# Optimization experiments

Hardware: AMD Instinct MI355X
Metric: run time of the kernel (lower is better)

The kernel has to match this reference:

```python
import jax, jax.numpy as jnp
import numpy as np
import math

DIM = 1024
HEADS = 16
SEQ_LEN = 2048
NUM_PV = 32
HEAD_DIM = DIM // HEADS
EPS = 1e-5


def setup_inputs() -> dict:
    key = jax.random.key(0)
    k1, k2 = jax.random.split(key)
    B = 4
    L = SEQ_LEN + NUM_PV
    x = jax.random.normal(k1, (B, L, DIM), dtype=jnp.float32)
    paramvecs = jax.random.normal(k2, (1, NUM_PV, DIM), dtype=jnp.float32)
    return {"x": x, "paramvecs": paramvecs}


def _layernorm_noaffine(x):
    mu = jnp.mean(x, axis=-1, keepdims=True)
    var = jnp.mean(jnp.square(x - mu), axis=-1, keepdims=True)
    return (x - mu) * jax.lax.rsqrt(var + EPS)


def reference(x, paramvecs):
    B, L, D = x.shape  # L = SEQ_LEN + NUM_PV
    # add learned param vectors onto the trailing num_paramvec positions
    x = x.at[:, SEQ_LEN:, :].add(paramvecs)
    residual = x
    xn = _layernorm_noaffine(x)
    # shared Q = K = V = xn, split into heads: [B, H, L, Dh]
    h = xn.reshape(B, L, HEADS, HEAD_DIM).transpose(0, 2, 1, 3)
    scores = jnp.einsum('bhqd,bhkd->bhqk', h, h) / math.sqrt(HEAD_DIM)
    weights = jax.nn.softmax(scores, axis=-1)
    context = jnp.einsum('bhqk,bhkd->bhqd', weights, h)
    context = context.transpose(0, 2, 1, 3).reshape(B, L, D)
    return context + residual
```

## Files before the change

### kernel.cpp

```cpp
#include <hip/hip_runtime.h>
#include <hip/hip_fp16.h>

#define DIMF 1024
#define NHEADS 16
#define SEQ 2048
#define NPV 32
#define HD 64
#define LTOT 2080
#define LP 2112
#define NB 4
#define BHN 64
#define NQT 33
#define QB 64
#define NQB 33
#define NKV 65

typedef _Float16 f16x8 __attribute__((ext_vector_type(8)));
typedef float f32x16 __attribute__((ext_vector_type(16)));
typedef unsigned short u16x8 __attribute__((ext_vector_type(8)));
typedef int v2i __attribute__((ext_vector_type(2)));

#if __has_builtin(__builtin_amdgcn_exp2f)
#define EXP2(x) __builtin_amdgcn_exp2f(x)
#else
#define EXP2(x) exp2f(x)
#endif

#define CEXP 0.1803368801111f
#define KSH  11.5415603271f

__global__ __launch_bounds__(256) void prep_kernel(const float* __restrict__ x,
                                                   const float* __restrict__ pv,
                                                   float* __restrict__ out,
                                                   unsigned short* __restrict__ xnh) {
  int row = blockIdx.x;
  int b = row / LP, l = row - b * LP;
  int t = threadIdx.x;
  int h = t >> 4;
  int dd = (t & 15) << 2;
  unsigned short* dst = xnh + ((size_t)(b * NHEADS + h) * LP + l) * HD + dd;
  if (l >= LTOT) {
    *reinterpret_cast<ushort4*>(dst) = make_ushort4(0, 0, 0, 0);
    return;
  }
  const float* xr = x + ((size_t)b * LTOT + l) * DIMF + t * 4;
  float4 v = *reinterpret_cast<const float4*>(xr);
  if (l >= SEQ) {
    float4 p = *reinterpret_cast<const float4*>(pv + (size_t)(l - SEQ) * DIMF + t * 4);
    v.x += p.x; v.y += p.y; v.z += p.z; v.w += p.w;
  }
  *reinterpret_cast<float4*>(out + ((size_t)b * LTOT + l) * DIMF + t * 4) = v;

  float s1 = v.x + v.y + v.z + v.w;
  float s2 = v.x * v.x + v.y * v.y + v.z * v.z + v.w * v.w;
#pragma unroll
  for (int o = 1; o < 64; o <<= 1) { s1 += __shfl_xor(s1, o); s2 += __shfl_xor(s2, o); }
  __shared__ float red[8];
  int wv = t >> 6;
  if ((t & 63) == 0) { red[wv] = s1; red[4 + wv] = s2; }
  __syncthreads();
  s1 = red[0] + red[1] + red[2] + red[3];
  s2 = red[4] + red[5] + red[6] + red[7];
  float mu = s1 * (1.0f / DIMF);
  float var = s2 * (1.0f / DIMF) - mu * mu;
  float rs = rsqrtf(var + 1e-5f);
  ushort4 o4;
  o4.x = __half_as_ushort(__float2half((v.x - mu) * rs));
  o4.y = __half_as_ushort(__float2half((v.y - mu) * rs));
  o4.z = __half_as_ushort(__float2half((v.z - mu) * rs));
  o4.w = __half_as_ushort(__float2half((v.w - mu) * rs));
  *reinterpret_cast<ushort4*>(dst) = o4;
}

__global__ __launch_bounds__(256) void transpose_kernel(const unsigned short* __restrict__ xnh,
                                                        unsigned short* __restrict__ xnt) {
  __shared__ unsigned short tile[64][72];
  int blk = blockIdx.x;
  int bh = blk / NQT, lt = blk - bh * NQT;
  int t = threadIdx.x;
  int rr = t >> 3;
  int c8 = (t & 7) << 3;
#pragma unroll
  for (int p = 0; p < 2; p++) {
    int ll = rr + p * 32;
    float4 v = *reinterpret_cast<const float4*>(xnh + ((size_t)bh * LP + lt * 64 + ll) * HD + c8);
    int cs = c8 ^ (((ll >> 3) & 7) << 3);
    *reinterpret_cast<float4*>(&tile[ll][cs]) = v;
  }
  __syncthreads();
  int l8 = (t & 7) << 3;
#pragma unroll
  for (int p = 0; p < 2; p++) {
    int d = rr + p * 32;
    u16x8 o;
#pragma unroll
    for (int j = 0; j < 8; j++) {
      o[j] = tile[l8 + j][d ^ ((t & 7) << 3)];
    }
    *reinterpret_cast<u16x8*>(xnt + ((size_t)bh * HD + d) * LP + lt * 64 + l8) = o;
  }
}

static __device__ __forceinline__ f32x16 mfma32(f16x8 a, f16x8 b, f32x16 c) {
  return __builtin_amdgcn_mfma_f32_32x32x16_f16(a, b, c, 0, 0, 0);
}

static __device__ __forceinline__ unsigned cvtpk(float a, float b) {
  auto h = __builtin_amdgcn_cvt_pkrtz(a, b);
  return __builtin_bit_cast(unsigned, h);
}

static __device__ __forceinline__ void pack2(const f32x16& P, f16x8& f0, f16x8& f1) {
  unsigned a0 = cvtpk(P[0], P[1]),  b0 = cvtpk(P[4], P[5]);
  unsigned a1 = cvtpk(P[2], P[3]),  b1 = cvtpk(P[6], P[7]);
  v2i s0 = __builtin_amdgcn_permlane32_swap(a0, b0, false, false);
  v2i s1 = __builtin_amdgcn_permlane32_swap(a1, b1, false, false);
  unsigned a2 = cvtpk(P[8], P[9]),   b2 = cvtpk(P[12], P[13]);
  unsigned a3 = cvtpk(P[10], P[11]), b3 = cvtpk(P[14], P[15]);
  v2i s2 = __builtin_amdgcn_permlane32_swap(a2, b2, false, false);
  v2i s3 = __builtin_amdgcn_permlane32_swap(a3, b3, false, false);
  union { unsigned u[4]; f16x8 v; } u0, u1;
  u0.u[0] = (unsigned)s0.x; u0.u[1] = (unsigned)s1.x; u0.u[2] = (unsigned)s0.y; u0.u[3] = (unsigned)s1.y;
  u1.u[0] = (unsigned)s2.x; u1.u[1] = (unsigned)s3.x; u1.u[2] = (unsigned)s2.y; u1.u[3] = (unsigned)s3.y;
  f0 = u0.v; f1 = u1.v;
}

#define GLDS(src, dst) \
  __builtin_amdgcn_global_load_lds( \
      (const __attribute__((address_space(1))) unsigned int*)(src), \
      (__attribute__((address_space(3))) unsigned int*)(dst), 16, 0, 0)

__device__ __forceinline__ void kv_step16(const unsigned short* kbuf, const unsigned short* vbuf,
                                          const f16x8 (&qf)[4], f32x16& accA, f32x16& accB,
                                          float& rowsum, int l31, int hi, int sw) {
  const unsigned short* k0 = kbuf + (size_t)l31 * 64;
  f32x16 st;
#pragma unroll
  for (int r = 0; r < 16; r++) st[r] = -KSH;
  __builtin_amdgcn_s_setprio(1);
#pragma unroll
  for (int ds = 0; ds < 4; ds++) {
    int cl = ds * 2 + hi;
    f16x8 ka = *reinterpret_cast<const f16x8*>(k0 + ((cl ^ sw) << 3));
    st = mfma32(ka, qf[ds], st);
  }
  __builtin_amdgcn_s_setprio(0);
#pragma unroll
  for (int r = 0; r < 16; r++) {
    st[r] = EXP2(st[r]);
    rowsum += st[r];
  }
  f16x8 pa[2];
  pack2(st, pa[0], pa[1]);
  const unsigned short* v0 = vbuf + (size_t)l31 * 64;
  __builtin_amdgcn_s_setprio(1);
#pragma unroll
  for (int ks = 0; ks < 2; ks++) {
    int clA = ks * 2 + hi;
    f16x8 bvA = *reinterpret_cast<const f16x8*>(v0 + ((clA ^ sw) << 3));
    accA = mfma32(pa[ks], bvA, accA);
    int clB = 4 + ks * 2 + hi;
    f16x8 bvB = *reinterpret_cast<const f16x8*>(v0 + ((clB ^ sw) << 3));
    accB = mfma32(pa[ks], bvB, accB);
  }
  __builtin_amdgcn_s_setprio(0);
}

__global__ __launch_bounds__(128, 4) void attn_kernel(const unsigned short* __restrict__ xnh,
                                                      const unsigned short* __restrict__ xnt,
                                                      float* __restrict__ out) {
  __shared__ unsigned short kt0[32 * 64], kt1[32 * 64];
  __shared__ unsigned short vt0[32 * 64], vt1[32 * 64];
  __shared__ float wred[2][32];
  int bid = blockIdx.x;
  const int nwg = BHN * NQB;
  const int cpx = nwg >> 3;
  int wg = (bid & 7) * cpx + (bid >> 3);
  int bh = wg / NQB, qt = wg - bh * NQB;
  int b = bh >> 4, h = bh & 15;
  int tid = threadIdx.x;
  int wid = tid >> 6;
  int lane = tid & 63;
  int l31 = lane & 31, hi = lane >> 5;
  int sw = l31 & 7;
  int q0w = qt * QB + wid * 32;
  const unsigned short* Kb = xnh + (size_t)bh * (LP * HD);
  const unsigned short* Vb = xnt + (size_t)bh * (HD * LP);

  f16x8 qf[4];
  const _Float16 ce = (_Float16)CEXP;
  const f16x8 cev = {ce, ce, ce, ce, ce, ce, ce, ce};
#pragma unroll
  for (int ds = 0; ds < 4; ds++) {
    qf[ds] = *reinterpret_cast<const f16x8*>(Kb + (size_t)(q0w + l31) * HD + ds * 16 + hi * 8);
    qf[ds] = qf[ds] * cev;
  }

  f32x16 accA = {};
  f32x16 accB = {};
  float rowsum = 0.f;

  int srow = tid >> 3;
  int scol = ((tid & 7) ^ (srow & 7)) << 3;
  const unsigned short* pK = Kb + (size_t)srow * HD + scol;
  int vcl = (tid & 7) ^ (srow & 7);
  const unsigned short* pV = Vb + (size_t)(srow + 32 * (vcl >> 2)) * LP + (vcl & 3) * 8;
  int wo = wid * 512;

#define STAGE(kb, vb) do { \
    GLDS(pK, (kb) + wo); GLDS(pK + 16 * HD, (kb) + 1024 + wo); \
    GLDS(pV, (vb) + wo); GLDS(pV + (size_t)16 * LP, (vb) + 1024 + wo); \
    pK += 32 * HD; pV += 32; } while (0)

  STAGE(kt0, vt0);
  __syncthreads();

  for (int it = 0; it < 32; ++it) {
    STAGE(kt1, vt1);
    kv_step16(kt0, vt0, qf, accA, accB, rowsum, l31, hi, sw);
    __syncthreads();
    STAGE(kt0, vt0);
    kv_step16(kt1, vt1, qf, accA, accB, rowsum, l31, hi, sw);
    __syncthreads();
  }
  kv_step16(kt0, vt0, qf, accA, accB, rowsum, l31, hi, sw);

  float full = rowsum + __shfl_xor(rowsum, 32);
  float inv = 1.0f / full;
  if (lane < 32) wred[wid][l31] = inv;
  float* obase = out + (size_t)b * LTOT * DIMF + h * HD + l31;
  if (q0w < LTOT) {
#pragma unroll
    for (int q2 = 0; q2 < 4; q2++) {
      float4 iv = *reinterpret_cast<const float4*>(&wred[wid][q2 * 8 + hi * 4]);
#pragma unroll
      for (int j = 0; j < 4; j++) {
        int qg = q0w + q2 * 8 + hi * 4 + j;
        float* p = obase + (size_t)qg * DIMF;
        float ivj = (j == 0) ? iv.x : (j == 1) ? iv.y : (j == 2) ? iv.z : iv.w;
        p[0]  += accA[q2 * 4 + j] * ivj;
        p[32] += accB[q2 * 4 + j] * ivj;
      }
    }
  }
#undef STAGE
}

extern "C" void kernel_launch(void* const* d_in, const int* in_sizes, int n_in,
                              void* d_out, int out_size, void* d_ws, size_t ws_size,
                              hipStream_t stream) {
  const float* x  = (const float*)d_in[0];
  const float* pv = (const float*)d_in[1];
  float* out = (float*)d_out;
  unsigned short* xnh = (unsigned short*)d_ws;
  unsigned short* xnt = xnh + (size_t)BHN * LP * HD;
  prep_kernel<<<NB * LP, 256, 0, stream>>>(x, pv, out, xnh);
  transpose_kernel<<<BHN * NQT, 256, 0, stream>>>(xnh, xnt);
  attn_kernel<<<BHN * NQB, 128, 0, stream>>>(xnh, xnt, out);
}
```

Baseline: 132.9 us.

## Process 64 query rows per single wave to reuse K/V fragments

The attention workgroup shrinks from two waves (32 queries each) to one wave that handles all 64 queries of the tile. Each K and V fragment read from LDS now feeds two sets of MFMAs, which halves LDS read traffic per query and gives the scheduler more independent MFMA work. The cost is higher register pressure from doubled accumulators and query fragments, and fewer waves per workgroup, which reduces latency hiding. The single wave also now issues all the global-to-LDS staging loads.

```diff
diff --git a/kernel.cpp b/kernel.cpp
--- a/kernel.cpp
+++ b/kernel.cpp
@@ -130,45 +130,55 @@
       (const __attribute__((address_space(1))) unsigned int*)(src), \
       (__attribute__((address_space(3))) unsigned int*)(dst), 16, 0, 0)
 
-__device__ __forceinline__ void kv_step16(const unsigned short* kbuf, const unsigned short* vbuf,
-                                          const f16x8 (&qf)[4], f32x16& accA, f32x16& accB,
-                                          float& rowsum, int l31, int hi, int sw) {
+__device__ __forceinline__ void kv_step64(const unsigned short* kbuf, const unsigned short* vbuf,
+                                          const f16x8 (&qf0)[4], const f16x8 (&qf1)[4],
+                                          f32x16& accA0, f32x16& accB0,
+                                          f32x16& accA1, f32x16& accB1,
+                                          float& rs0, float& rs1, int l31, int hi, int sw) {
   const unsigned short* k0 = kbuf + (size_t)l31 * 64;
-  f32x16 st;
-#pragma unroll
-  for (int r = 0; r < 16; r++) st[r] = -KSH;
-  __builtin_amdgcn_s_setprio(1);
+  f16x8 ka[4];
 #pragma unroll
   for (int ds = 0; ds < 4; ds++) {
     int cl = ds * 2 + hi;
-    f16x8 ka = *reinterpret_cast<const f16x8*>(k0 + ((cl ^ sw) << 3));
-    st = mfma32(ka, qf[ds], st);
-  }
+    ka[ds] = *reinterpret_cast<const f16x8*>(k0 + ((cl ^ sw) << 3));
+  }
+  f32x16 st0, st1;
+#pragma unroll
+  for (int r = 0; r < 16; r++) { st0[r] = -KSH; st1[r] = -KSH; }
+  __builtin_amdgcn_s_setprio(1);
+#pragma unroll
+  for (int ds = 0; ds < 4; ds++) st0 = mfma32(ka[ds], qf0[ds], st0);
+#pragma unroll
+  for (int ds = 0; ds < 4; ds++) st1 = mfma32(ka[ds], qf1[ds], st1);
   __builtin_amdgcn_s_setprio(0);
 #pragma unroll
-  for (int r = 0; r < 16; r++) {
-    st[r] = EXP2(st[r]);
-    rowsum += st[r];
-  }
-  f16x8 pa[2];
-  pack2(st, pa[0], pa[1]);
+  for (int r = 0; r < 16; r++) { st0[r] = EXP2(st0[r]); rs0 += st0[r]; }
+  f16x8 pa0[2], pa1[2];
+  pack2(st0, pa0[0], pa0[1]);
+#pragma unroll
+  for (int r = 0; r < 16; r++) { st1[r] = EXP2(st1[r]); rs1 += st1[r]; }
+  pack2(st1, pa1[0], pa1[1]);
   const unsigned short* v0 = vbuf + (size_t)l31 * 64;
+  f16x8 bvA[2], bvB[2];
+#pragma unroll
+  for (int ks = 0; ks < 2; ks++) {
+    bvA[ks] = *reinterpret_cast<const f16x8*>(v0 + (((ks * 2 + hi) ^ sw) << 3));
+    bvB[ks] = *reinterpret_cast<const f16x8*>(v0 + (((4 + ks * 2 + hi) ^ sw) << 3));
+  }
   __builtin_amdgcn_s_setprio(1);
 #pragma unroll
   for (int ks = 0; ks < 2; ks++) {
-    int clA = ks * 2 + hi;
-    f16x8 bvA = *reinterpret_cast<const f16x8*>(v0 + ((clA ^ sw) << 3));
-    accA = mfma32(pa[ks], bvA, accA);
-    int clB = 4 + ks * 2 + hi;
-    f16x8 bvB = *reinterpret_cast<const f16x8*>(v0 + ((clB ^ sw) << 3));
-    accB = mfma32(pa[ks], bvB, accB);
+    accA0 = mfma32(pa0[ks], bvA[ks], accA0);
+    accB0 = mfma32(pa0[ks], bvB[ks], accB0);
+    accA1 = mfma32(pa1[ks], bvA[ks], accA1);
+    accB1 = mfma32(pa1[ks], bvB[ks], accB1);
   }
   __builtin_amdgcn_s_setprio(0);
 }
 
-__global__ __launch_bounds__(128, 4) void attn_kernel(const unsigned short* __restrict__ xnh,
-                                                      const unsigned short* __restrict__ xnt,
-                                                      float* __restrict__ out) {
+__global__ __launch_bounds__(64, 2) void attn_kernel(const unsigned short* __restrict__ xnh,
+                                                     const unsigned short* __restrict__ xnt,
+                                                     float* __restrict__ out) {
   __shared__ unsigned short kt0[32 * 64], kt1[32 * 64];
   __shared__ unsigned short vt0[32 * 64], vt1[32 * 64];
   __shared__ float wred[2][32];
@@ -178,68 +188,88 @@
   int wg = (bid & 7) * cpx + (bid >> 3);
   int bh = wg / NQB, qt = wg - bh * NQB;
   int b = bh >> 4, h = bh & 15;
-  int tid = threadIdx.x;
-  int wid = tid >> 6;
-  int lane = tid & 63;
+  int lane = threadIdx.x;
   int l31 = lane & 31, hi = lane >> 5;
   int sw = l31 & 7;
-  int q0w = qt * QB + wid * 32;
+  int q0 = qt * QB;
   const unsigned short* Kb = xnh + (size_t)bh * (LP * HD);
   const unsigned short* Vb = xnt + (size_t)bh * (HD * LP);
 
-  f16x8 qf[4];
+  f16x8 qf0[4], qf1[4];
   const _Float16 ce = (_Float16)CEXP;
   const f16x8 cev = {ce, ce, ce, ce, ce, ce, ce, ce};
 #pragma unroll
   for (int ds = 0; ds < 4; ds++) {
-    qf[ds] = *reinterpret_cast<const f16x8*>(Kb + (size_t)(q0w + l31) * HD + ds * 16 + hi * 8);
-    qf[ds] = qf[ds] * cev;
-  }
-
-  f32x16 accA = {};
-  f32x16 accB = {};
-  float rowsum = 0.f;
-
-  int srow = tid >> 3;
-  int scol = ((tid & 7) ^ (srow & 7)) << 3;
-  const unsigned short* pK = Kb + (size_t)srow * HD + scol;
-  int vcl = (tid & 7) ^ (srow & 7);
-  const unsigned short* pV = Vb + (size_t)(srow + 32 * (vcl >> 2)) * LP + (vcl & 3) * 8;
-  int wo = wid * 512;
+    qf0[ds] = *reinterpret_cast<const f16x8*>(Kb + (size_t)(q0 + l31) * HD + ds * 16 + hi * 8);
+    qf0[ds] = qf0[ds] * cev;
+    qf1[ds] = *reinterpret_cast<const f16x8*>(Kb + (size_t)(q0 + 32 + l31) * HD + ds * 16 + hi * 8);
+    qf1[ds] = qf1[ds] * cev;
+  }
+
+  f32x16 accA0 = {}, accB0 = {};
+  f32x16 accA1 = {}, accB1 = {};
+  float rs0 = 0.f, rs1 = 0.f;
+
+  int krow8 = lane >> 3;
+  int kcol = ((lane & 7) ^ (krow8 & 7)) << 3;
+  const unsigned short* pK0 = Kb + (size_t)krow8 * HD + kcol;
+  const unsigned short* pK1 = pK0 + 8 * HD;
+  const unsigned short* pK2 = pK0 + 16 * HD;
+  const unsigned short* pK3 = pK0 + 24 * HD;
+  int vcl = (lane & 7) ^ (krow8 & 7);
+  const unsigned short* pV0 = Vb + (size_t)(krow8 + 32 * (vcl >> 2)) * LP + (vcl & 3) * 8;
+  const unsigned short* pV1 = pV0 + (size_t)8 * LP;
+  const unsigned short* pV2 = pV0 + (size_t)16 * LP;
+  const unsigned short* pV3 = pV0 + (size_t)24 * LP;
 
 #define STAGE(kb, vb) do { \
-    GLDS(pK, (kb) + wo); GLDS(pK + 16 * HD, (kb) + 1024 + wo); \
-    GLDS(pV, (vb) + wo); GLDS(pV + (size_t)16 * LP, (vb) + 1024 + wo); \
-    pK += 32 * HD; pV += 32; } while (0)
+    GLDS(pK0, (kb));        GLDS(pK1, (kb) + 512); \
+    GLDS(pK2, (kb) + 1024); GLDS(pK3, (kb) + 1536); \
+    GLDS(pV0, (vb));        GLDS(pV1, (vb) + 512); \
+    GLDS(pV2, (vb) + 1024); GLDS(pV3, (vb) + 1536); \
+    pK0 += 32 * HD; pK1 += 32 * HD; pK2 += 32 * HD; pK3 += 32 * HD; \
+    pV0 += 32; pV1 += 32; pV2 += 32; pV3 += 32; } while (0)
 
   STAGE(kt0, vt0);
   __syncthreads();
 
   for (int it = 0; it < 32; ++it) {
     STAGE(kt1, vt1);
-    kv_step16(kt0, vt0, qf, accA, accB, rowsum, l31, hi, sw);
+    kv_step64(kt0, vt0, qf0, qf1, accA0, accB0, accA1, accB1, rs0, rs1, l31, hi, sw);
     __syncthreads();
     STAGE(kt0, vt0);
-    kv_step16(kt1, vt1, qf, accA, accB, rowsum, l31, hi, sw);
+    kv_step64(kt1, vt1, qf0, qf1, accA0, accB0, accA1, accB1, rs0, rs1, l31, hi, sw);
     __syncthreads();
   }
-  kv_step16(kt0, vt0, qf, accA, accB, rowsum, l31, hi, sw);
-
-  float full = rowsum + __shfl_xor(rowsum, 32);
-  float inv = 1.0f / full;
-  if (lane < 32) wred[wid][l31] = inv;
+  kv_step64(kt0, vt0, qf0, qf1, accA0, accB0, accA1, accB1, rs0, rs1, l31, hi, sw);
+
+  float full0 = rs0 + __shfl_xor(rs0, 32);
+  float full1 = rs1 + __shfl_xor(rs1, 32);
+  if (lane < 32) { wred[0][l31] = 1.0f / full0; wred[1][l31] = 1.0f / full1; }
   float* obase = out + (size_t)b * LTOT * DIMF + h * HD + l31;
-  if (q0w < LTOT) {
+#pragma unroll
+  for (int q2 = 0; q2 < 4; q2++) {
+    float4 iv = *reinterpret_cast<const float4*>(&wred[0][q2 * 8 + hi * 4]);
+#pragma unroll
+    for (int j = 0; j < 4; j++) {
+      int qg = q0 + q2 * 8 + hi * 4 + j;
+      float* p = obase + (size_t)qg * DIMF;
+      float ivj = (j == 0) ? iv.x : (j == 1) ? iv.y : (j == 2) ? iv.z : iv.w;
+      p[0]  += accA0[q2 * 4 + j] * ivj;
+      p[32] += accB0[q2 * 4 + j] * ivj;
+    }
+  }
+  if (q0 + 32 < LTOT) {
 #pragma unroll
     for (int q2 = 0; q2 < 4; q2++) {
-      float4 iv = *reinterpret_cast<const float4*>(&wred[wid][q2 * 8 + hi * 4]);
+      float4 iv = *reinterpret_cast<const float4*>(&wred[1][q2 * 8 + hi * 4]);
 #pragma unroll
       for (int j = 0; j < 4; j++) {
-        int qg = q0w + q2 * 8 + hi * 4 + j;
+        int qg = q0 + 32 + q2 * 8 + hi * 4 + j;
         float* p = obase + (size_t)qg * DIMF;
         float ivj = (j == 0) ? iv.x : (j == 1) ? iv.y : (j == 2) ? iv.z : iv.w;
-        p[0]  += accA[q2 * 4 + j] * ivj;
-        p[32] += accB[q2 * 4 + j] * ivj;
+        p[0]  += accA1[q2 * 4 + j] * ivj;
+        p[32] += accB1[q2 * 4 + j] * ivj;
       }
     }
   }
@@ -256,5 +286,5 @@
   unsigned short* xnt = xnh + (size_t)BHN * LP * HD;
   prep_kernel<<<NB * LP, 256, 0, stream>>>(x, pv, out, xnh);
   transpose_kernel<<<BHN * NQT, 256, 0, stream>>>(xnh, xnt);
-  attn_kernel<<<BHN * NQB, 128, 0, stream>>>(xnh, xnt, out);
-}
+  attn_kernel<<<BHN * NQB, 64, 0, stream>>>(xnh, xnt, out);
+}
```

New measurement: 137.8 us. +3.7%, slower.
